# Optimization experiments

Measured on AMD Instinct MI355X. Metric: run time of the kernel, lower is better.

The kernel has to match this reference:

```python
import jax, jax.numpy as jnp
import numpy as np

INF = 10000.0
HEAD_SIZE = 64
HEADS = 12


def _rope_tables(seqlen, dim, dtype=jnp.float32):
    inv_freq = 1.0 / (10000.0 ** (jnp.arange(0, dim, 2, dtype=dtype) / dim))
    t = jnp.arange(seqlen, dtype=dtype)
    freqs = t[:, None] * inv_freq[None, :]  # [n, dim//2]
    return jnp.sin(freqs), jnp.cos(freqs)


def _apply_rope(t, sin, cos):
    # t: [b, n, d]; sin/cos: [n, d//2]
    t1, t2 = t[..., 0::2], t[..., 1::2]
    r1 = t1 * cos - t2 * sin
    r2 = t1 * sin + t2 * cos
    return jnp.stack([r1, r2], axis=-1).reshape(t.shape)


def setup_inputs() -> dict:
    key = jax.random.key(0)
    k1, k2, k3, k4, k5, k6 = jax.random.split(key, 6)
    B, N, H = 16, 512, 1024
    inputs = jax.random.normal(k1, (B, N, H), dtype=jnp.float32)
    attention_mask = jax.random.randint(k2, (B, N), 0, 2, dtype=jnp.int32)
    w1 = jax.random.normal(k3, (H, 2 * HEAD_SIZE), dtype=jnp.float32) * 0.02
    b1 = jax.random.normal(k4, (2 * HEAD_SIZE,), dtype=jnp.float32) * 0.02
    w2 = jax.random.normal(k5, (2 * HEAD_SIZE, 2 * HEADS), dtype=jnp.float32) * 0.02
    b2 = jax.random.normal(k6, (2 * HEADS,), dtype=jnp.float32) * 0.02
    return {"inputs": inputs, "attention_mask": attention_mask,
            "w1": w1, "b1": b1, "w2": w2, "b2": b2}


def reference(inputs, attention_mask, w1, b1, w2, b2):
    B, N, _ = inputs.shape
    x = inputs @ w1 + b1  # [b, n, 2*head_size]
    qw, kw = x[..., 0::2], x[..., 1::2]  # each [b, n, head_size]
    sin, cos = _rope_tables(N, HEAD_SIZE, x.dtype)
    qw = _apply_rope(qw, sin, cos)
    kw = _apply_rope(kw, sin, cos)
    logits = jnp.einsum('bmd,bnd->bmn', qw, kw) / (HEAD_SIZE ** 0.5)
    bias = jnp.swapaxes(x @ w2 + b2, 1, 2) / 2.0  # [b, 2*heads, n]
    logits = logits[:, None] + bias[:, 0::2, None, :] + bias[:, 1::2, :, None]  # [b, h, m, n]
    am = attention_mask.astype(logits.dtype)
    pad_mask = 1.0 - am[:, None, None, :] * am[:, None, :, None]
    logits = logits - pad_mask * INF
    idx = jnp.arange(N)
    tril = (idx[:, None] > idx[None, :]).astype(logits.dtype)  # strict lower triangle
    logits = logits - tril * INF
    return logits
```

## Files before the change

kernel.cpp:

```cpp
#include <hip/hip_runtime.h>

typedef __bf16 bf16_t;
typedef bf16_t bf16x4 __attribute__((ext_vector_type(4)));
typedef bf16_t bf16x8 __attribute__((ext_vector_type(8)));
typedef float f32x4 __attribute__((ext_vector_type(4)));

#define INFV 10000.0f

__global__ __launch_bounds__(256) void k0_transpose(const float* __restrict__ w1,
                                                    bf16_t* __restrict__ w1T) {
    __shared__ float s[32][36];
    const int t = threadIdx.x;
    const int k0 = (blockIdx.x & 31) * 32;
    const int c0 = (blockIdx.x >> 5) * 32;
    {
        const int r = t >> 3, cc = (t & 7) * 4;
        *(float4*)&s[r][cc] = *(const float4*)&w1[(size_t)(k0 + r) * 128 + c0 + cc];
    }
    __syncthreads();
    {
        const int cr = t >> 3, kk = (t & 7) * 4;
        bf16x4 v;
        v[0] = (bf16_t)s[kk + 0][cr];
        v[1] = (bf16_t)s[kk + 1][cr];
        v[2] = (bf16_t)s[kk + 2][cr];
        v[3] = (bf16_t)s[kk + 3][cr];
        *(bf16x4*)&w1T[(size_t)(c0 + cr) * 1024 + k0 + kk] = v;
    }
}

__global__ __launch_bounds__(256) void k1_proj(
    const float* __restrict__ inputs,
    const bf16_t* __restrict__ w1T,
    const float* __restrict__ b1,
    const float* __restrict__ w2,
    const float* __restrict__ b2,
    bf16_t* __restrict__ qg,
    bf16_t* __restrict__ kg,
    float* __restrict__ biasT)
{
    __shared__ bf16_t s_a[32][72];
    __shared__ float s_x[32][132];
    __shared__ float s_w2T[24][132];

    const int t = threadIdx.x;
    const int row0 = blockIdx.x * 32;
    const int lane = t & 63, wave = t >> 6;
    const int wm = wave >> 1, wn = wave & 1;
    const int cn = lane & 15, kgrp = lane >> 4;

    for (int i = t; i < 3072; i += 256) {
        int j = i / 24, c = i - j * 24;
        s_w2T[c][j] = w2[i];
    }

    f32x4 acc[4] = {};
    const int sr0 = t >> 4, sc0 = (t & 15) * 4;
    const int sr1 = 16 + sr0;
    float4 pf0 = *(const float4*)&inputs[(size_t)(row0 + sr0) * 1024 + sc0];
    float4 pf1 = *(const float4*)&inputs[(size_t)(row0 + sr1) * 1024 + sc0];

    for (int ks = 0; ks < 16; ++ks) {
        const int k0 = ks * 64;
        {
            bf16x4 v0, v1;
            v0[0] = (bf16_t)pf0.x; v0[1] = (bf16_t)pf0.y; v0[2] = (bf16_t)pf0.z; v0[3] = (bf16_t)pf0.w;
            v1[0] = (bf16_t)pf1.x; v1[1] = (bf16_t)pf1.y; v1[2] = (bf16_t)pf1.z; v1[3] = (bf16_t)pf1.w;
            *(bf16x4*)&s_a[sr0][sc0] = v0;
            *(bf16x4*)&s_a[sr1][sc0] = v1;
        }
        __syncthreads();
        if (ks < 15) {
            pf0 = *(const float4*)&inputs[(size_t)(row0 + sr0) * 1024 + k0 + 64 + sc0];
            pf1 = *(const float4*)&inputs[(size_t)(row0 + sr1) * 1024 + k0 + 64 + sc0];
        }
        const int arow = wm * 16 + cn;
        bf16x8 a0 = *(const bf16x8*)&s_a[arow][kgrp * 8];
        bf16x8 a1 = *(const bf16x8*)&s_a[arow][32 + kgrp * 8];
#pragma unroll
        for (int tt = 0; tt < 4; ++tt) {
            const int col = wn * 64 + tt * 16 + cn;
            const bf16_t* wp = w1T + (size_t)col * 1024 + k0 + kgrp * 8;
            bf16x8 bb0 = *(const bf16x8*)wp;
            bf16x8 bb1 = *(const bf16x8*)(wp + 32);
            acc[tt] = __builtin_amdgcn_mfma_f32_16x16x32_bf16(a0, bb0, acc[tt], 0, 0, 0);
            acc[tt] = __builtin_amdgcn_mfma_f32_16x16x32_bf16(a1, bb1, acc[tt], 0, 0, 0);
        }
        __syncthreads();
    }

    {
        const int rgrp = lane >> 4;
#pragma unroll
        for (int tt = 0; tt < 4; ++tt) {
            const int col = wn * 64 + tt * 16 + cn;
            const float bb = b1[col];
#pragma unroll
            for (int r = 0; r < 4; ++r)
                s_x[wm * 16 + rgrp * 4 + r][col] = acc[tt][r] + bb;
        }
    }
    __syncthreads();

    {
        const int r = t >> 3;
        const int i0 = (t & 7) * 4;
        const int rowg = row0 + r;
        const int n = rowg & 511;
        bf16x8 qv, kv;
#pragma unroll
        for (int u = 0; u < 4; ++u) {
            const int i = i0 + u;
            float fr = (float)n * exp2f((float)i * -0.4152410118609203f);
            float sv, cv;
            sincosf(fr, &sv, &cv);
            float x0 = s_x[r][4 * i + 0];
            float x1 = s_x[r][4 * i + 1];
            float x2 = s_x[r][4 * i + 2];
            float x3 = s_x[r][4 * i + 3];
            qv[2 * u]     = (bf16_t)(x0 * cv - x2 * sv);
            qv[2 * u + 1] = (bf16_t)(x0 * sv + x2 * cv);
            kv[2 * u]     = (bf16_t)(x1 * cv - x3 * sv);
            kv[2 * u + 1] = (bf16_t)(x1 * sv + x3 * cv);
        }
        *(bf16x8*)&qg[(size_t)rowg * 64 + 2 * i0] = qv;
        *(bf16x8*)&kg[(size_t)rowg * 64 + 2 * i0] = kv;
    }

    {
        const int r = t >> 3;
        const int cb = (t & 7) * 3;
        float sum0 = 0.f, sum1 = 0.f, sum2 = 0.f;
#pragma unroll 4
        for (int j = 0; j < 128; j += 4) {
            float4 xv = *(const float4*)&s_x[r][j];
            float4 wa = *(const float4*)&s_w2T[cb + 0][j];
            float4 wb = *(const float4*)&s_w2T[cb + 1][j];
            float4 wc = *(const float4*)&s_w2T[cb + 2][j];
            sum0 += xv.x * wa.x + xv.y * wa.y + xv.z * wa.z + xv.w * wa.w;
            sum1 += xv.x * wb.x + xv.y * wb.y + xv.z * wb.z + xv.w * wb.w;
            sum2 += xv.x * wc.x + xv.y * wc.y + xv.z * wc.z + xv.w * wc.w;
        }
        const int rowg = row0 + r;
        const int bb = rowg >> 9, n = rowg & 511;
        float* bp = biasT + (size_t)bb * 12288 + n;
        bp[(size_t)(cb + 0) * 512] = (sum0 + b2[cb + 0]) * 0.5f;
        bp[(size_t)(cb + 1) * 512] = (sum1 + b2[cb + 1]) * 0.5f;
        bp[(size_t)(cb + 2) * 512] = (sum2 + b2[cb + 2]) * 0.5f;
    }
}

__global__ __launch_bounds__(256) void k2_logits(
    const bf16_t* __restrict__ qg, const bf16_t* __restrict__ kg,
    const float* __restrict__ biasT, const int* __restrict__ am,
    float* __restrict__ out)
{
    __shared__ float s_be[12][64], s_bo[12][64];
    __shared__ float s_pm[64], s_pn[64];

    const int t = threadIdx.x;
    const int b = blockIdx.z;
    const int m0 = blockIdx.y * 64;
    const int n0 = blockIdx.x * 64;

    for (int i = t; i < 768; i += 256) {
        const int h = i >> 6, j = i & 63;
        s_be[h][j] = biasT[(size_t)b * 12288 + (size_t)(2 * h) * 512 + n0 + j];
        s_bo[h][j] = biasT[(size_t)b * 12288 + (size_t)(2 * h + 1) * 512 + m0 + j];
    }
    if (t < 64) s_pm[t] = (float)am[b * 512 + m0 + t];
    else if (t < 128) s_pn[t - 64] = (float)am[b * 512 + n0 + (t - 64)];

    const int lane = t & 63, wave = t >> 6;
    const int cn = lane & 15, kgrp = lane >> 4;

    const bf16_t* qp = qg + ((size_t)(b * 512 + m0 + wave * 16 + cn)) * 64 + kgrp * 8;
    bf16x8 a0 = *(const bf16x8*)qp;
    bf16x8 a1 = *(const bf16x8*)(qp + 32);

    f32x4 acc[4] = {};
#pragma unroll
    for (int nt = 0; nt < 4; ++nt) {
        const bf16_t* kp = kg + ((size_t)(b * 512 + n0 + nt * 16 + cn)) * 64 + kgrp * 8;
        bf16x8 bb0 = *(const bf16x8*)kp;
        bf16x8 bb1 = *(const bf16x8*)(kp + 32);
        acc[nt] = __builtin_amdgcn_mfma_f32_16x16x32_bf16(a0, bb0, acc[nt], 0, 0, 0);
        acc[nt] = __builtin_amdgcn_mfma_f32_16x16x32_bf16(a1, bb1, acc[nt], 0, 0, 0);
    }
    __syncthreads();

    const int rgrp = lane >> 4;
#pragma unroll
    for (int nt = 0; nt < 4; ++nt) {
        const int n = nt * 16 + cn;
        const float an = s_pn[n];
#pragma unroll
        for (int rg = 0; rg < 4; ++rg) {
            const int m = wave * 16 + rgrp * 4 + rg;
            float v = acc[nt][rg] * 0.125f;
            v -= (1.0f - s_pm[m] * an) * INFV;
            if (m0 + m > n0 + n) v -= INFV;
            acc[nt][rg] = v;
        }
    }

    float* ob = out + (size_t)b * 3145728 + (size_t)m0 * 512 + n0;
    for (int h = 0; h < 12; ++h) {
#pragma unroll
        for (int nt = 0; nt < 4; ++nt) {
            const int n = nt * 16 + cn;
            const float be = s_be[h][n];
#pragma unroll
            for (int rg = 0; rg < 4; ++rg) {
                const int m = wave * 16 + rgrp * 4 + rg;
                ob[(size_t)h * 262144 + (size_t)m * 512 + n] = acc[nt][rg] + be + s_bo[h][m];
            }
        }
    }
}

extern "C" void kernel_launch(void* const* d_in, const int* in_sizes, int n_in,
                              void* d_out, int out_size, void* d_ws, size_t ws_size,
                              hipStream_t stream) {
    const float* inputs = (const float*)d_in[0];
    const int*   am     = (const int*)d_in[1];
    const float* w1     = (const float*)d_in[2];
    const float* b1     = (const float*)d_in[3];
    const float* w2     = (const float*)d_in[4];
    const float* b2     = (const float*)d_in[5];
    float* out = (float*)d_out;

    bf16_t* w1T   = (bf16_t*)d_ws;
    bf16_t* qg    = w1T + 131072;
    bf16_t* kg    = qg + 524288;
    float*  biasT = (float*)(kg + 524288);

    k0_transpose<<<128, 256, 0, stream>>>(w1, w1T);
    k1_proj<<<256, 256, 0, stream>>>(inputs, w1T, b1, w2, b2, qg, kg, biasT);
    k2_logits<<<dim3(8, 8, 16), 256, 0, stream>>>(qg, kg, biasT, am, out);
}
```

Before: 71.99 us.

## Swap MFMA operands for row-contiguous vector stores and halve projection tile rows

The logits kernel now passes K as the A operand and Q as the B operand, so each lane holds four consecutive n values for a single m row. The 12-head output write therefore becomes 16-byte vector stores instead of scalar strided stores, which is meant to cut store instruction count and improve coalescing on the dominant output write. Separately, the projection kernel drops to 16 rows per block with 512 blocks to spread work across more CUs. The cost is that each block reloads w1T and w2 twice as often and some threads sit idle in the bias step.

```diff
diff --git a/kernel.cpp b/kernel.cpp
--- a/kernel.cpp
+++ b/kernel.cpp
@@ -39,14 +39,13 @@
     bf16_t* __restrict__ kg,
     float* __restrict__ biasT)
 {
-    __shared__ bf16_t s_a[32][72];
-    __shared__ float s_x[32][132];
+    __shared__ bf16_t s_a[16][72];
+    __shared__ float s_x[16][132];
     __shared__ float s_w2T[24][132];
 
     const int t = threadIdx.x;
-    const int row0 = blockIdx.x * 32;
+    const int row0 = blockIdx.x * 16;
     const int lane = t & 63, wave = t >> 6;
-    const int wm = wave >> 1, wn = wave & 1;
     const int cn = lane & 15, kgrp = lane >> 4;
 
     for (int i = t; i < 3072; i += 256) {
@@ -54,32 +53,26 @@
         s_w2T[c][j] = w2[i];
     }
 
-    f32x4 acc[4] = {};
-    const int sr0 = t >> 4, sc0 = (t & 15) * 4;
-    const int sr1 = 16 + sr0;
-    float4 pf0 = *(const float4*)&inputs[(size_t)(row0 + sr0) * 1024 + sc0];
-    float4 pf1 = *(const float4*)&inputs[(size_t)(row0 + sr1) * 1024 + sc0];
+    f32x4 acc[2] = {};
+    const int sr = t >> 4;
+    const int sc = (t & 15) * 4;
+    float4 pf = *(const float4*)&inputs[(size_t)(row0 + sr) * 1024 + sc];
 
     for (int ks = 0; ks < 16; ++ks) {
         const int k0 = ks * 64;
         {
-            bf16x4 v0, v1;
-            v0[0] = (bf16_t)pf0.x; v0[1] = (bf16_t)pf0.y; v0[2] = (bf16_t)pf0.z; v0[3] = (bf16_t)pf0.w;
-            v1[0] = (bf16_t)pf1.x; v1[1] = (bf16_t)pf1.y; v1[2] = (bf16_t)pf1.z; v1[3] = (bf16_t)pf1.w;
-            *(bf16x4*)&s_a[sr0][sc0] = v0;
-            *(bf16x4*)&s_a[sr1][sc0] = v1;
+            bf16x4 v;
+            v[0] = (bf16_t)pf.x; v[1] = (bf16_t)pf.y; v[2] = (bf16_t)pf.z; v[3] = (bf16_t)pf.w;
+            *(bf16x4*)&s_a[sr][sc] = v;
         }
         __syncthreads();
-        if (ks < 15) {
-            pf0 = *(const float4*)&inputs[(size_t)(row0 + sr0) * 1024 + k0 + 64 + sc0];
-            pf1 = *(const float4*)&inputs[(size_t)(row0 + sr1) * 1024 + k0 + 64 + sc0];
-        }
-        const int arow = wm * 16 + cn;
-        bf16x8 a0 = *(const bf16x8*)&s_a[arow][kgrp * 8];
-        bf16x8 a1 = *(const bf16x8*)&s_a[arow][32 + kgrp * 8];
-#pragma unroll
-        for (int tt = 0; tt < 4; ++tt) {
-            const int col = wn * 64 + tt * 16 + cn;
+        if (ks < 15)
+            pf = *(const float4*)&inputs[(size_t)(row0 + sr) * 1024 + k0 + 64 + sc];
+        bf16x8 a0 = *(const bf16x8*)&s_a[cn][kgrp * 8];
+        bf16x8 a1 = *(const bf16x8*)&s_a[cn][32 + kgrp * 8];
+#pragma unroll
+        for (int tt = 0; tt < 2; ++tt) {
+            const int col = wave * 32 + tt * 16 + cn;
             const bf16_t* wp = w1T + (size_t)col * 1024 + k0 + kgrp * 8;
             bf16x8 bb0 = *(const bf16x8*)wp;
             bf16x8 bb1 = *(const bf16x8*)(wp + 32);
@@ -92,24 +85,24 @@
     {
         const int rgrp = lane >> 4;
 #pragma unroll
-        for (int tt = 0; tt < 4; ++tt) {
-            const int col = wn * 64 + tt * 16 + cn;
+        for (int tt = 0; tt < 2; ++tt) {
+            const int col = wave * 32 + tt * 16 + cn;
             const float bb = b1[col];
 #pragma unroll
             for (int r = 0; r < 4; ++r)
-                s_x[wm * 16 + rgrp * 4 + r][col] = acc[tt][r] + bb;
+                s_x[rgrp * 4 + r][col] = acc[tt][r] + bb;
         }
     }
     __syncthreads();
 
     {
-        const int r = t >> 3;
-        const int i0 = (t & 7) * 4;
+        const int r = t >> 4;
+        const int i0 = (t & 15) * 2;
         const int rowg = row0 + r;
         const int n = rowg & 511;
-        bf16x8 qv, kv;
-#pragma unroll
-        for (int u = 0; u < 4; ++u) {
+        bf16x4 qv, kv;
+#pragma unroll
+        for (int u = 0; u < 2; ++u) {
             const int i = i0 + u;
             float fr = (float)n * exp2f((float)i * -0.4152410118609203f);
             float sv, cv;
@@ -123,30 +116,30 @@
             kv[2 * u]     = (bf16_t)(x1 * cv - x3 * sv);
             kv[2 * u + 1] = (bf16_t)(x1 * sv + x3 * cv);
         }
-        *(bf16x8*)&qg[(size_t)rowg * 64 + 2 * i0] = qv;
-        *(bf16x8*)&kg[(size_t)rowg * 64 + 2 * i0] = kv;
-    }
-
-    {
-        const int r = t >> 3;
-        const int cb = (t & 7) * 3;
-        float sum0 = 0.f, sum1 = 0.f, sum2 = 0.f;
+        *(bf16x4*)&qg[(size_t)rowg * 64 + 2 * i0] = qv;
+        *(bf16x4*)&kg[(size_t)rowg * 64 + 2 * i0] = kv;
+    }
+
+    {
+        const int r = t >> 4;
+        const int cb = t & 15;
+        if (cb < 12) {
+            const int c0 = cb * 2;
+            float sum0 = 0.f, sum1 = 0.f;
 #pragma unroll 4
-        for (int j = 0; j < 128; j += 4) {
-            float4 xv = *(const float4*)&s_x[r][j];
-            float4 wa = *(const float4*)&s_w2T[cb + 0][j];
-            float4 wb = *(const float4*)&s_w2T[cb + 1][j];
-            float4 wc = *(const float4*)&s_w2T[cb + 2][j];
-            sum0 += xv.x * wa.x + xv.y * wa.y + xv.z * wa.z + xv.w * wa.w;
-            sum1 += xv.x * wb.x + xv.y * wb.y + xv.z * wb.z + xv.w * wb.w;
-            sum2 += xv.x * wc.x + xv.y * wc.y + xv.z * wc.z + xv.w * wc.w;
-        }
-        const int rowg = row0 + r;
-        const int bb = rowg >> 9, n = rowg & 511;
-        float* bp = biasT + (size_t)bb * 12288 + n;
-        bp[(size_t)(cb + 0) * 512] = (sum0 + b2[cb + 0]) * 0.5f;
-        bp[(size_t)(cb + 1) * 512] = (sum1 + b2[cb + 1]) * 0.5f;
-        bp[(size_t)(cb + 2) * 512] = (sum2 + b2[cb + 2]) * 0.5f;
+            for (int j = 0; j < 128; j += 4) {
+                float4 xv = *(const float4*)&s_x[r][j];
+                float4 wa = *(const float4*)&s_w2T[c0 + 0][j];
+                float4 wb = *(const float4*)&s_w2T[c0 + 1][j];
+                sum0 += xv.x * wa.x + xv.y * wa.y + xv.z * wa.z + xv.w * wa.w;
+                sum1 += xv.x * wb.x + xv.y * wb.y + xv.z * wb.z + xv.w * wb.w;
+            }
+            const int rowg = row0 + r;
+            const int bb = rowg >> 9, n = rowg & 511;
+            float* bp = biasT + (size_t)bb * 12288 + n;
+            bp[(size_t)(c0 + 0) * 512] = (sum0 + b2[c0 + 0]) * 0.5f;
+            bp[(size_t)(c0 + 1) * 512] = (sum1 + b2[c0 + 1]) * 0.5f;
+        }
     }
 }
 
@@ -175,46 +168,47 @@
     const int cn = lane & 15, kgrp = lane >> 4;
 
     const bf16_t* qp = qg + ((size_t)(b * 512 + m0 + wave * 16 + cn)) * 64 + kgrp * 8;
-    bf16x8 a0 = *(const bf16x8*)qp;
-    bf16x8 a1 = *(const bf16x8*)(qp + 32);
+    bf16x8 qb0 = *(const bf16x8*)qp;
+    bf16x8 qb1 = *(const bf16x8*)(qp + 32);
 
     f32x4 acc[4] = {};
 #pragma unroll
     for (int nt = 0; nt < 4; ++nt) {
         const bf16_t* kp = kg + ((size_t)(b * 512 + n0 + nt * 16 + cn)) * 64 + kgrp * 8;
-        bf16x8 bb0 = *(const bf16x8*)kp;
-        bf16x8 bb1 = *(const bf16x8*)(kp + 32);
-        acc[nt] = __builtin_amdgcn_mfma_f32_16x16x32_bf16(a0, bb0, acc[nt], 0, 0, 0);
-        acc[nt] = __builtin_amdgcn_mfma_f32_16x16x32_bf16(a1, bb1, acc[nt], 0, 0, 0);
+        bf16x8 ka0 = *(const bf16x8*)kp;
+        bf16x8 ka1 = *(const bf16x8*)(kp + 32);
+        acc[nt] = __builtin_amdgcn_mfma_f32_16x16x32_bf16(ka0, qb0, acc[nt], 0, 0, 0);
+        acc[nt] = __builtin_amdgcn_mfma_f32_16x16x32_bf16(ka1, qb1, acc[nt], 0, 0, 0);
     }
     __syncthreads();
 
     const int rgrp = lane >> 4;
+    const int m_loc = wave * 16 + cn;
+    const int m = m0 + m_loc;
+    const float am_m = s_pm[m_loc];
+
 #pragma unroll
     for (int nt = 0; nt < 4; ++nt) {
-        const int n = nt * 16 + cn;
-        const float an = s_pn[n];
-#pragma unroll
-        for (int rg = 0; rg < 4; ++rg) {
-            const int m = wave * 16 + rgrp * 4 + rg;
-            float v = acc[nt][rg] * 0.125f;
-            v -= (1.0f - s_pm[m] * an) * INFV;
-            if (m0 + m > n0 + n) v -= INFV;
-            acc[nt][rg] = v;
-        }
-    }
-
-    float* ob = out + (size_t)b * 3145728 + (size_t)m0 * 512 + n0;
+#pragma unroll
+        for (int r = 0; r < 4; ++r) {
+            const int n_loc = nt * 16 + rgrp * 4 + r;
+            float v = acc[nt][r] * 0.125f;
+            v -= (1.0f - am_m * s_pn[n_loc]) * INFV;
+            if (m > n0 + n_loc) v -= INFV;
+            acc[nt][r] = v;
+        }
+    }
+
+    float* ob = out + (size_t)b * 3145728 + (size_t)m * 512 + n0;
+#pragma unroll
     for (int h = 0; h < 12; ++h) {
+        const float bo = s_bo[h][m_loc];
+        const f32x4 bov = {bo, bo, bo, bo};
 #pragma unroll
         for (int nt = 0; nt < 4; ++nt) {
-            const int n = nt * 16 + cn;
-            const float be = s_be[h][n];
-#pragma unroll
-            for (int rg = 0; rg < 4; ++rg) {
-                const int m = wave * 16 + rgrp * 4 + rg;
-                ob[(size_t)h * 262144 + (size_t)m * 512 + n] = acc[nt][rg] + be + s_bo[h][m];
-            }
+            const f32x4 be4 = *(const f32x4*)&s_be[h][nt * 16 + rgrp * 4];
+            f32x4 w = acc[nt] + be4 + bov;
+            *(f32x4*)&ob[(size_t)h * 262144 + nt * 16 + rgrp * 4] = w;
         }
     }
 }
@@ -236,6 +230,6 @@
     float*  biasT = (float*)(kg + 524288);
 
     k0_transpose<<<128, 256, 0, stream>>>(w1, w1T);
-    k1_proj<<<256, 256, 0, stream>>>(inputs, w1T, b1, w2, b2, qg, kg, biasT);
+    k1_proj<<<512, 256, 0, stream>>>(inputs, w1T, b1, w2, b2, qg, kg, biasT);
     k2_logits<<<dim3(8, 8, 16), 256, 0, stream>>>(qg, kg, biasT, am, out);
 }
```

Result: faster. 67.71 us (-5.9%).
